# Performance work log

Hardware: AMD Instinct MI355X
Metric: run time of the kernel (lower is better)

The kernel has to match this reference:

```python
import jax, jax.numpy as jnp
import numpy as np

B, T, C, H = 4, 2048, 1024, 16
HD = C // H  # head dim = 64


def _rope(x, pos):
    """Rotary embedding. x: [B,H,T,hd], pos: [B,T] int positions."""
    half = x.shape[-1] // 2
    inv_freq = 1.0 / (10000.0 ** (jnp.arange(half, dtype=jnp.float32) / half))
    ang = pos.astype(jnp.float32)[:, None, :, None] * inv_freq  # [B,1,T,half]
    cos, sin = jnp.cos(ang), jnp.sin(ang)
    x1, x2 = x[..., :half], x[..., half:]
    return jnp.concatenate([x1 * cos - x2 * sin, x1 * sin + x2 * cos], axis=-1)


def setup_inputs() -> dict:
    key = jax.random.key(0)
    k1, k2, k3 = jax.random.split(key, 3)
    x = jax.random.normal(k1, (B, T, C), dtype=jnp.float32)
    W_attn = jax.random.normal(k2, (C, 3 * C), dtype=jnp.float32) * (1.0 / np.sqrt(C))
    W_proj = jax.random.normal(k3, (C, C), dtype=jnp.float32) * (1.0 / np.sqrt(C))
    indices = jnp.broadcast_to(jnp.arange(T, dtype=jnp.int32)[None, :], (B, T))
    return {"x": x, "W_attn": W_attn, "W_proj": W_proj, "indices": indices}


def reference(x, W_attn, W_proj, indices):
    # QKV projection (bias=False)
    qkv = x @ W_attn  # [B,T,3C]
    q, k, v = jnp.split(qkv, 3, axis=-1)

    def to_heads(t):
        return t.reshape(B, T, H, HD).transpose(0, 2, 1, 3)  # [B,H,T,hd]

    q, k, v = to_heads(q), to_heads(k), to_heads(v)
    # RoPE on q and k at positions given by indices (pos_emb_closure.adapt_*)
    q = _rope(q, indices)
    k = _rope(k, indices)

    # attn_mask = k_indices <= q_indices, shape [B,1,T,T]
    mask = indices[:, None, None, :] <= indices[:, None, :, None]

    att = jnp.einsum("bhqd,bhkd->bhqk", q, k) * (1.0 / np.sqrt(HD))
    att = jnp.where(mask, att, jnp.float32(-jnp.inf))
    att = jax.nn.softmax(att, axis=-1)
    y = jnp.einsum("bhqk,bhkd->bhqd", att, v)  # [B,H,T,hd]
    y = y.transpose(0, 2, 1, 3).reshape(B, T, C)
    return y @ W_proj
```

## Files before the change

kernel.cpp:

```cpp
#include <hip/hip_runtime.h>
#include <math.h>

namespace {
constexpr int Bsz = 4;
constexpr int T   = 2048;
constexpr int C   = 1024;
constexpr int H   = 16;
constexpr int HD  = 64;

typedef short bf16x8 __attribute__((ext_vector_type(8)));
typedef float f32x4  __attribute__((ext_vector_type(4)));
typedef unsigned int u32x4 __attribute__((ext_vector_type(4)));

#if defined(__has_builtin)
#if __has_builtin(__builtin_amdgcn_global_load_lds)
#define HAVE_GLL 1
typedef __attribute__((address_space(3))) unsigned int lds_u32_t;
typedef __attribute__((address_space(1))) unsigned int g_u32_t;
#define GLL16(gp, lp)                                                        \
  __builtin_amdgcn_global_load_lds((const g_u32_t*)(gp), (lds_u32_t*)(lp),   \
                                   16, 0, 0)
#endif
#endif

__device__ __forceinline__ unsigned short f2bf(float f) {
  unsigned int u = __builtin_bit_cast(unsigned int, f);
  u += 0x7FFFu + ((u >> 16) & 1u);
  return (unsigned short)(u >> 16);
}
__device__ __forceinline__ unsigned int cvtpk_bf16(float a, float b) {
  unsigned int r;
  asm("v_cvt_pk_bf16_f32 %0, %1, %2" : "=v"(r) : "v"(a), "v"(b));
  return r;
}

__global__ __launch_bounds__(256) void f32_to_bf16_kernel(
    const float* __restrict__ in, unsigned short* __restrict__ out, int n4) {
  int i = blockIdx.x * 256 + threadIdx.x;
  if (i < n4) {
    float4 v = ((const float4*)in)[i];
    ushort4 o;
    o.x = f2bf(v.x); o.y = f2bf(v.y); o.z = f2bf(v.z); o.w = f2bf(v.w);
    ((ushort4*)out)[i] = o;
  }
}

__global__ __launch_bounds__(256) void transpose_bf16_kernel(
    const float* __restrict__ W, unsigned short* __restrict__ Wt, int K, int N) {
  __shared__ float tile[32][33];
  const int n0 = blockIdx.x * 32, k0 = blockIdx.y * 32;
  const int r = threadIdx.x >> 3, c4 = threadIdx.x & 7;
  float4 v = *(const float4*)(W + (size_t)(k0 + r) * N + n0 + c4 * 4);
  tile[r][c4 * 4 + 0] = v.x;
  tile[r][c4 * 4 + 1] = v.y;
  tile[r][c4 * 4 + 2] = v.z;
  tile[r][c4 * 4 + 3] = v.w;
  __syncthreads();
  ushort4 o;
  o.x = f2bf(tile[c4 * 4 + 0][r]);
  o.y = f2bf(tile[c4 * 4 + 1][r]);
  o.z = f2bf(tile[c4 * 4 + 2][r]);
  o.w = f2bf(tile[c4 * 4 + 3][r]);
  *(ushort4*)(Wt + (size_t)(n0 + r) * K + k0 + c4 * 4) = o;
}

__global__ __launch_bounds__(256) void rope_table_kernel(
    const int* __restrict__ idx, float2* __restrict__ tab) {
  const int i = blockIdx.x * 256 + threadIdx.x;
  const int d = i & 31, g = i >> 5;
  const int pos = idx[g];
  const float inv = exp2f((float)d * -0.41524101186f);
  float sn, cs;
  sincosf((float)pos * inv, &sn, &cs);
  tab[i] = make_float2(cs, sn);
}

template <int MODE>
__global__ __launch_bounds__(256) void gemm_bt(
    const unsigned short* __restrict__ A, const unsigned short* __restrict__ Bt,
    float* __restrict__ Cout, unsigned short* __restrict__ qp,
    unsigned short* __restrict__ kp, unsigned short* __restrict__ vp,
    const float2* __restrict__ tab, int M, int N, int K) {
  __shared__ __align__(16) unsigned short As[128 * 32];
  __shared__ __align__(16) unsigned short Bs[128 * 32];
  const int tid = threadIdx.x;
  const int lane = tid & 63, w = tid >> 6;
  const int wr = w & 1, wc = w >> 1;
  const int l15 = lane & 15, quad = lane >> 4;
  const int m0 = blockIdx.y * 128, n0 = blockIdx.x * 128;

  const int srow = lane >> 2;
  const int schunk = (lane & 3) * 8;
  const unsigned short* gA = A + (size_t)(m0 + w * 32 + srow) * K + schunk;
  const unsigned short* gB = Bt + (size_t)(n0 + w * 32 + srow) * K + schunk;
  unsigned short* lA0 = &As[(w * 32) * 32 + lane * 8];
  unsigned short* lA1 = &As[(w * 32 + 16) * 32 + lane * 8];
  unsigned short* lB0 = &Bs[(w * 32) * 32 + lane * 8];
  unsigned short* lB1 = &Bs[(w * 32 + 16) * 32 + lane * 8];

  f32x4 acc[4][4] = {};

  for (int k0 = 0; k0 < K; k0 += 32) {
    __syncthreads();
#ifdef HAVE_GLL
    GLL16(gA + k0, lA0);
    GLL16(gA + (size_t)16 * K + k0, lA1);
    GLL16(gB + k0, lB0);
    GLL16(gB + (size_t)16 * K + k0, lB1);
#else
    *(uint4*)lA0 = *(const uint4*)(gA + k0);
    *(uint4*)lA1 = *(const uint4*)(gA + (size_t)16 * K + k0);
    *(uint4*)lB0 = *(const uint4*)(gB + k0);
    *(uint4*)lB1 = *(const uint4*)(gB + (size_t)16 * K + k0);
#endif
    __syncthreads();

    bf16x8 af[4], bfr[4];
#pragma unroll
    for (int mf = 0; mf < 4; ++mf)
      af[mf] = *(const bf16x8*)&As[(wr * 64 + mf * 16 + l15) * 32 + quad * 8];
#pragma unroll
    for (int nf = 0; nf < 4; ++nf)
      bfr[nf] = *(const bf16x8*)&Bs[(wc * 64 + nf * 16 + l15) * 32 + quad * 8];
#pragma unroll
    for (int mf = 0; mf < 4; ++mf)
#pragma unroll
      for (int nf = 0; nf < 4; ++nf)
        acc[mf][nf] = __builtin_amdgcn_mfma_f32_16x16x32_bf16(
            af[mf], bfr[nf], acc[mf][nf], 0, 0, 0);
  }

  if (MODE == 0) {
#pragma unroll
    for (int mf = 0; mf < 4; ++mf) {
      const int row0 = m0 + wr * 64 + mf * 16 + quad * 4;
#pragma unroll
      for (int nf = 0; nf < 4; ++nf) {
        const int col = n0 + wc * 64 + nf * 16 + l15;
#pragma unroll
        for (int r = 0; r < 4; ++r)
          Cout[(size_t)(row0 + r) * N + col] = acc[mf][nf][r];
      }
    }
  } else {
    const int colbase = n0 + wc * 64;
    const int which = colbase >> 10;
    if (which == 2) {
#pragma unroll
      for (int mf = 0; mf < 4; ++mf) {
        const int row0 = m0 + wr * 64 + mf * 16 + quad * 4;
        const int b = row0 >> 11, t0 = row0 & (T - 1);
#pragma unroll
        for (int nf = 0; nf < 4; ++nf) {
          const int rem = (colbase + nf * 16 + l15) & (C - 1);
          const int h = rem >> 6, hd = rem & 63;
          ushort4 pv;
          pv.x = f2bf(acc[mf][nf][0]);
          pv.y = f2bf(acc[mf][nf][1]);
          pv.z = f2bf(acc[mf][nf][2]);
          pv.w = f2bf(acc[mf][nf][3]);
          *(ushort4*)(vp + (((size_t)(b * H + h)) * HD + hd) * T + t0) = pv;
        }
      }
    } else {
      unsigned short* dst = (which == 0) ? qp : kp;
      const float sc = (which == 0) ? 0.18033688f : 1.0f;
      const int h = ((colbase + l15) & (C - 1)) >> 6;
#pragma unroll
      for (int mf = 0; mf < 4; ++mf) {
        const int row0 = m0 + wr * 64 + mf * 16 + quad * 4;
        const int b = row0 >> 11, t0 = row0 & (T - 1);
        const size_t obase = ((size_t)(b * H + h)) * T + t0;
        const float2* tb = tab + ((size_t)(b * T + t0) << 5);
#pragma unroll
        for (int nf = 0; nf < 2; ++nf) {
          const int d = nf * 16 + l15;
#pragma unroll
          for (int r = 0; r < 4; ++r) {
            const float2 cssn = tb[(r << 5) + d];
            const float x1 = acc[mf][nf][r], x2 = acc[mf][nf + 2][r];
            dst[(obase + r) * HD + d]      = f2bf((x1 * cssn.x - x2 * cssn.y) * sc);
            dst[(obase + r) * HD + d + 32] = f2bf((x1 * cssn.y + x2 * cssn.x) * sc);
          }
        }
      }
    }
  }
}

__global__ __launch_bounds__(256) void flash_attn_mfma(
    const unsigned short* __restrict__ q, const unsigned short* __restrict__ k,
    const unsigned short* __restrict__ vt, const int* __restrict__ idx,
    unsigned short* __restrict__ y) {
  __shared__ __align__(16) unsigned short Ks[2][64 * 64];
  __shared__ __align__(16) unsigned short Vts[2][64 * 64];

  const int tid = threadIdx.x;
  const int lane = tid & 63, w = tid >> 6;
  const int l15 = lane & 15, quad = lane >> 4;

  const int flat = (blockIdx.z * H + blockIdx.y) * 32 + blockIdx.x;
  const int slot = flat >> 3;
  const int bh_i = (flat & 7) * 8 + (slot >> 5);
  const int qt = 31 - (slot & 31);
  const int h = bh_i & (H - 1), b = bh_i >> 4;

  const size_t bh = (size_t)bh_i;
  const unsigned short* qg = q + bh * T * HD;
  const unsigned short* kg = k + bh * T * HD;
  const unsigned short* vg = vt + bh * HD * T;
  const int* idxb = idx + b * T;

  int km;
  {
    const int4* p4 = (const int4*)(idxb + (lane << 5));
    int4 v0 = p4[0];
    int m = max(max(v0.x, v0.y), max(v0.z, v0.w));
#pragma unroll
    for (int j = 1; j < 8; ++j) {
      int4 v = p4[j];
      m = max(m, max(max(v.x, v.y), max(v.z, v.w)));
    }
    km = max(m, __shfl_xor(m, 1));
  }

  const int r1 = tid >> 3, c1 = tid & 7;
  const int r2 = r1 + 32;
  const int xr1 = (r1 & 7) << 3;
  const int swS1 = r1 * 64 + ((c1 * 8) ^ xr1);
  const int swS2 = r2 * 64 + ((c1 * 8) ^ xr1);
  const int vbase = 32 * (c1 >> 2) + 16 * (c1 & 1) + 4 * ((c1 >> 1) & 1);
  const int vo1a = r1 * 64 + ((vbase + 0) ^ xr1);
  const int vo1b = r1 * 64 + ((vbase + 8) ^ xr1);
  const int vo2a = r2 * 64 + ((vbase + 0) ^ xr1);
  const int vo2b = r2 * 64 + ((vbase + 8) ^ xr1);
  const int rx = (l15 & 7) << 3;

  const int qrow = qt * 64 + w * 16 + l15;

  const bf16x8 bq0 = *(const bf16x8*)(qg + (size_t)qrow * HD + quad * 8);
  const bf16x8 bq1 = *(const bf16x8*)(qg + (size_t)qrow * HD + 32 + quad * 8);
  const int pq = idxb[qrow];
  int mq = pq;
  mq = min(mq, __shfl_xor(mq, 1));
  mq = min(mq, __shfl_xor(mq, 2));
  mq = min(mq, __shfl_xor(mq, 4));
  mq = min(mq, __shfl_xor(mq, 8));
  const unsigned long long bal = __ballot(km > mq);

  float m_run = -1e38f, lq = 0.0f;
  f32x4 Oa[4] = {};

  {
    uint4 ka = *(const uint4*)(kg + (size_t)r1 * HD + c1 * 8);
    uint4 kb = *(const uint4*)(kg + (size_t)r2 * HD + c1 * 8);
    uint4 va = *(const uint4*)(vg + (size_t)r1 * T + c1 * 8);
    uint4 vb = *(const uint4*)(vg + (size_t)r2 * T + c1 * 8);
    *(uint4*)&Ks[0][swS1] = ka;
    *(uint4*)&Ks[0][swS2] = kb;
    *(uint2*)&Vts[0][vo1a] = make_uint2(va.x, va.y);
    *(uint2*)&Vts[0][vo1b] = make_uint2(va.z, va.w);
    *(uint2*)&Vts[0][vo2a] = make_uint2(vb.x, vb.y);
    *(uint2*)&Vts[0][vo2b] = make_uint2(vb.z, vb.w);
  }

  for (int kt = 0; kt <= qt; ++kt) {
    const int cur = kt & 1;
    const int k0 = kt * 64;
    __syncthreads();

    uint4 nka, nkb, nva, nvb;
    if (kt < qt) {
      const int kn = k0 + 64;
      nka = *(const uint4*)(kg + (size_t)(kn + r1) * HD + c1 * 8);
      nkb = *(const uint4*)(kg + (size_t)(kn + r2) * HD + c1 * 8);
      nva = *(const uint4*)(vg + (size_t)r1 * T + kn + c1 * 8);
      nvb = *(const uint4*)(vg + (size_t)r2 * T + kn + c1 * 8);
    }

    f32x4 Sa[4];
    __builtin_amdgcn_s_setprio(1);
#pragma unroll
    for (int nf = 0; nf < 4; ++nf) {
      const int row = (nf * 16 + l15) * 64;
      bf16x8 ak0 = *(const bf16x8*)&Ks[cur][row + ((quad * 8) ^ rx)];
      bf16x8 ak1 = *(const bf16x8*)&Ks[cur][row + ((32 + quad * 8) ^ rx)];
      f32x4 s = {};
      s = __builtin_amdgcn_mfma_f32_16x16x32_bf16(ak0, bq0, s, 0, 0, 0);
      s = __builtin_amdgcn_mfma_f32_16x16x32_bf16(ak1, bq1, s, 0, 0, 0);
      Sa[nf] = s;
    }
    __builtin_amdgcn_s_setprio(0);

    if ((bal >> (kt + kt)) & 1ull) {
#pragma unroll
      for (int nf = 0; nf < 4; ++nf) {
        const int4 pk4 = *(const int4*)(idxb + k0 + nf * 16 + quad * 4);
        if (pk4.x > pq) Sa[nf][0] = -3e38f;
        if (pk4.y > pq) Sa[nf][1] = -3e38f;
        if (pk4.z > pq) Sa[nf][2] = -3e38f;
        if (pk4.w > pq) Sa[nf][3] = -3e38f;
      }
    }

    float mx = fmaxf(
        fmaxf(fmaxf(fmaxf(Sa[0][0], Sa[0][1]), Sa[0][2]),
              fmaxf(fmaxf(Sa[0][3], Sa[1][0]), Sa[1][1])),
        fmaxf(fmaxf(fmaxf(Sa[1][2], Sa[1][3]), Sa[2][0]),
              fmaxf(fmaxf(Sa[2][1], Sa[2][2]), Sa[2][3])));
    mx = fmaxf(mx, fmaxf(fmaxf(Sa[3][0], Sa[3][1]), fmaxf(Sa[3][2], Sa[3][3])));
    mx = fmaxf(mx, __shfl_xor(mx, 16));
    mx = fmaxf(mx, __shfl_xor(mx, 32));

    if (!__all(mx <= m_run + 8.0f)) {
      const float mn = fmaxf(m_run, mx);
      const float alpha = exp2f(m_run - mn);
      m_run = mn;
      lq *= alpha;
#pragma unroll
      for (int nfd = 0; nfd < 4; ++nfd)
#pragma unroll
        for (int r = 0; r < 4; ++r) Oa[nfd][r] *= alpha;
    }

    u32x4 w0, w1;
#pragma unroll
    for (int nf = 0; nf < 4; ++nf) {
      float p0 = exp2f(Sa[nf][0] - m_run);
      float p1 = exp2f(Sa[nf][1] - m_run);
      float p2 = exp2f(Sa[nf][2] - m_run);
      float p3 = exp2f(Sa[nf][3] - m_run);
      Sa[nf][0] = p0; Sa[nf][1] = p1; Sa[nf][2] = p2; Sa[nf][3] = p3;
      if (nf < 2) {
        w0[nf * 2 + 0] = cvtpk_bf16(p0, p1);
        w0[nf * 2 + 1] = cvtpk_bf16(p2, p3);
      } else {
        w1[(nf - 2) * 2 + 0] = cvtpk_bf16(p0, p1);
        w1[(nf - 2) * 2 + 1] = cvtpk_bf16(p2, p3);
      }
    }
    const bf16x8 bp0 = __builtin_bit_cast(bf16x8, w0);
    const bf16x8 bp1 = __builtin_bit_cast(bf16x8, w1);

    __builtin_amdgcn_s_setprio(1);
#pragma unroll
    for (int nfd = 0; nfd < 4; ++nfd) {
      const int vrow = (nfd * 16 + l15) * 64;
      bf16x8 av0 = *(const bf16x8*)&Vts[cur][vrow + ((quad * 8) ^ rx)];
      bf16x8 av1 = *(const bf16x8*)&Vts[cur][vrow + ((32 + quad * 8) ^ rx)];
      Oa[nfd] = __builtin_amdgcn_mfma_f32_16x16x32_bf16(av0, bp0, Oa[nfd], 0, 0, 0);
      Oa[nfd] = __builtin_amdgcn_mfma_f32_16x16x32_bf16(av1, bp1, Oa[nfd], 0, 0, 0);
    }
    __builtin_amdgcn_s_setprio(0);

    lq += ((Sa[0][0] + Sa[0][1]) + (Sa[0][2] + Sa[0][3])) +
          ((Sa[1][0] + Sa[1][1]) + (Sa[1][2] + Sa[1][3])) +
          ((Sa[2][0] + Sa[2][1]) + (Sa[2][2] + Sa[2][3])) +
          ((Sa[3][0] + Sa[3][1]) + (Sa[3][2] + Sa[3][3]));

    if (kt < qt) {
      const int nxt = cur ^ 1;
      *(uint4*)&Ks[nxt][swS1] = nka;
      *(uint4*)&Ks[nxt][swS2] = nkb;
      *(uint2*)&Vts[nxt][vo1a] = make_uint2(nva.x, nva.y);
      *(uint2*)&Vts[nxt][vo1b] = make_uint2(nva.z, nva.w);
      *(uint2*)&Vts[nxt][vo2a] = make_uint2(nvb.x, nvb.y);
      *(uint2*)&Vts[nxt][vo2b] = make_uint2(nvb.z, nvb.w);
    }
  }

  float lsum = lq;
  lsum += __shfl_xor(lsum, 16);
  lsum += __shfl_xor(lsum, 32);
  const float rl = 1.0f / lsum;
  const size_t base = ((size_t)b * T + qrow) * (size_t)C + h * HD;
#pragma unroll
  for (int nfd = 0; nfd < 4; ++nfd) {
    ushort4 o;
    o.x = f2bf(Oa[nfd][0] * rl);
    o.y = f2bf(Oa[nfd][1] * rl);
    o.z = f2bf(Oa[nfd][2] * rl);
    o.w = f2bf(Oa[nfd][3] * rl);
    *(ushort4*)(y + base + nfd * 16 + quad * 4) = o;
  }
}

}

extern "C" void kernel_launch(void* const* d_in, const int* in_sizes, int n_in,
                              void* d_out, int out_size, void* d_ws,
                              size_t ws_size, hipStream_t stream) {
  const float* x      = (const float*)d_in[0];
  const float* W_attn = (const float*)d_in[1];
  const float* W_proj = (const float*)d_in[2];
  const int* indices  = (const int*)d_in[3];
  float* out = (float*)d_out;

  const size_t nM = (size_t)Bsz * T * C;
  unsigned short* xb  = (unsigned short*)d_ws;
  unsigned short* wat = xb + nM;
  unsigned short* wpt = wat + (size_t)3 * C * C;
  unsigned short* qp  = wpt + (size_t)C * C;
  unsigned short* kp  = qp + nM;
  unsigned short* vp  = kp + nM;
  unsigned short* yb  = vp + nM;
  float2* rtab = (float2*)(yb + nM);

  f32_to_bf16_kernel<<<(int)(nM / 4 / 256), 256, 0, stream>>>(x, xb, (int)(nM / 4));
  transpose_bf16_kernel<<<dim3(3 * C / 32, C / 32), 256, 0, stream>>>(W_attn, wat, C, 3 * C);
  transpose_bf16_kernel<<<dim3(C / 32, C / 32), 256, 0, stream>>>(W_proj, wpt, C, C);
  rope_table_kernel<<<(Bsz * T * 32) / 256, 256, 0, stream>>>(indices, rtab);
  gemm_bt<1><<<dim3(3 * C / 128, Bsz * T / 128), 256, 0, stream>>>(
      xb, wat, nullptr, qp, kp, vp, rtab, Bsz * T, 3 * C, C);
  flash_attn_mfma<<<dim3(32, H, Bsz), 256, 0, stream>>>(qp, kp, vp, indices, yb);
  gemm_bt<0><<<dim3(C / 128, Bsz * T / 128), 256, 0, stream>>>(
      yb, wpt, out, nullptr, nullptr, nullptr, nullptr, Bsz * T, C, C);
}
```

Before: 310.9 us.

## Load K fragments directly from global into registers, bypassing LDS

In the attention kernel, K tiles are no longer staged through shared memory. Each wave now loads its MFMA K operand fragments straight from global memory into registers and prefetches the next tile into a second register set. This removes the K LDS writes and reads and halves LDS usage. In exchange, every one of the four waves loads the full K tile separately, four times the global/L2 traffic for K, and register pressure rises by 16 extra VGPRs per set.

```diff
diff --git a/kernel.cpp b/kernel.cpp
--- a/kernel.cpp
+++ b/kernel.cpp
@@ -192,7 +192,6 @@
     const unsigned short* __restrict__ q, const unsigned short* __restrict__ k,
     const unsigned short* __restrict__ vt, const int* __restrict__ idx,
     unsigned short* __restrict__ y) {
-  __shared__ __align__(16) unsigned short Ks[2][64 * 64];
   __shared__ __align__(16) unsigned short Vts[2][64 * 64];
 
   const int tid = threadIdx.x;
@@ -227,8 +226,6 @@
   const int r1 = tid >> 3, c1 = tid & 7;
   const int r2 = r1 + 32;
   const int xr1 = (r1 & 7) << 3;
-  const int swS1 = r1 * 64 + ((c1 * 8) ^ xr1);
-  const int swS2 = r2 * 64 + ((c1 * 8) ^ xr1);
   const int vbase = 32 * (c1 >> 2) + 16 * (c1 & 1) + 4 * ((c1 >> 1) & 1);
   const int vo1a = r1 * 64 + ((vbase + 0) ^ xr1);
   const int vo1b = r1 * 64 + ((vbase + 8) ^ xr1);
@@ -248,16 +245,20 @@
   mq = min(mq, __shfl_xor(mq, 8));
   const unsigned long long bal = __ballot(km > mq);
 
+  const unsigned short* kfb = kg + (size_t)l15 * HD + quad * 8;
+
   float m_run = -1e38f, lq = 0.0f;
   f32x4 Oa[4] = {};
 
+  bf16x8 kc[8];
   {
-    uint4 ka = *(const uint4*)(kg + (size_t)r1 * HD + c1 * 8);
-    uint4 kb = *(const uint4*)(kg + (size_t)r2 * HD + c1 * 8);
+#pragma unroll
+    for (int nf = 0; nf < 4; ++nf) {
+      kc[nf * 2 + 0] = *(const bf16x8*)(kfb + (size_t)(nf * 16) * HD);
+      kc[nf * 2 + 1] = *(const bf16x8*)(kfb + (size_t)(nf * 16) * HD + 32);
+    }
     uint4 va = *(const uint4*)(vg + (size_t)r1 * T + c1 * 8);
     uint4 vb = *(const uint4*)(vg + (size_t)r2 * T + c1 * 8);
-    *(uint4*)&Ks[0][swS1] = ka;
-    *(uint4*)&Ks[0][swS2] = kb;
     *(uint2*)&Vts[0][vo1a] = make_uint2(va.x, va.y);
     *(uint2*)&Vts[0][vo1b] = make_uint2(va.z, va.w);
     *(uint2*)&Vts[0][vo2a] = make_uint2(vb.x, vb.y);
@@ -269,25 +270,27 @@
     const int k0 = kt * 64;
     __syncthreads();
 
-    uint4 nka, nkb, nva, nvb;
+    bf16x8 kn[8];
+    uint4 nva, nvb;
     if (kt < qt) {
-      const int kn = k0 + 64;
-      nka = *(const uint4*)(kg + (size_t)(kn + r1) * HD + c1 * 8);
-      nkb = *(const uint4*)(kg + (size_t)(kn + r2) * HD + c1 * 8);
-      nva = *(const uint4*)(vg + (size_t)r1 * T + kn + c1 * 8);
-      nvb = *(const uint4*)(vg + (size_t)r2 * T + kn + c1 * 8);
+      const int knext0 = k0 + 64;
+      const unsigned short* kfn = kfb + (size_t)knext0 * HD;
+#pragma unroll
+      for (int nf = 0; nf < 4; ++nf) {
+        kn[nf * 2 + 0] = *(const bf16x8*)(kfn + (size_t)(nf * 16) * HD);
+        kn[nf * 2 + 1] = *(const bf16x8*)(kfn + (size_t)(nf * 16) * HD + 32);
+      }
+      nva = *(const uint4*)(vg + (size_t)r1 * T + knext0 + c1 * 8);
+      nvb = *(const uint4*)(vg + (size_t)r2 * T + knext0 + c1 * 8);
     }
 
     f32x4 Sa[4];
     __builtin_amdgcn_s_setprio(1);
 #pragma unroll
     for (int nf = 0; nf < 4; ++nf) {
-      const int row = (nf * 16 + l15) * 64;
-      bf16x8 ak0 = *(const bf16x8*)&Ks[cur][row + ((quad * 8) ^ rx)];
-      bf16x8 ak1 = *(const bf16x8*)&Ks[cur][row + ((32 + quad * 8) ^ rx)];
       f32x4 s = {};
-      s = __builtin_amdgcn_mfma_f32_16x16x32_bf16(ak0, bq0, s, 0, 0, 0);
-      s = __builtin_amdgcn_mfma_f32_16x16x32_bf16(ak1, bq1, s, 0, 0, 0);
+      s = __builtin_amdgcn_mfma_f32_16x16x32_bf16(kc[nf * 2 + 0], bq0, s, 0, 0, 0);
+      s = __builtin_amdgcn_mfma_f32_16x16x32_bf16(kc[nf * 2 + 1], bq1, s, 0, 0, 0);
       Sa[nf] = s;
     }
     __builtin_amdgcn_s_setprio(0);
@@ -360,12 +363,12 @@
 
     if (kt < qt) {
       const int nxt = cur ^ 1;
-      *(uint4*)&Ks[nxt][swS1] = nka;
-      *(uint4*)&Ks[nxt][swS2] = nkb;
       *(uint2*)&Vts[nxt][vo1a] = make_uint2(nva.x, nva.y);
       *(uint2*)&Vts[nxt][vo1b] = make_uint2(nva.z, nva.w);
       *(uint2*)&Vts[nxt][vo2a] = make_uint2(nvb.x, nvb.y);
       *(uint2*)&Vts[nxt][vo2b] = make_uint2(nvb.z, nvb.w);
+#pragma unroll
+      for (int i = 0; i < 8; ++i) kc[i] = kn[i];
     }
   }
 
```

New measurement: 397.0 us. 27.7% more time.

## Process two 64-key tiles per iteration in flash attention loop

Applied to the files above, without the earlier changes.

The attention inner loop now handles 128 keys per iteration, two 64-wide subtiles sharing one barrier, one online-softmax max/rescale step, and one double-buffered prefetch of the next two tiles. Prefetch loads are issued after the QK and softmax max stage instead of at loop start. The aim is to halve barriers and rescale checks per key and to expose more independent MFMA work. The cost is double the LDS footprint (64KB), more live registers, and partial waste when qt is even and the second subtile is absent.

```diff
diff --git a/kernel.cpp b/kernel.cpp
--- a/kernel.cpp
+++ b/kernel.cpp
@@ -192,8 +192,8 @@
     const unsigned short* __restrict__ q, const unsigned short* __restrict__ k,
     const unsigned short* __restrict__ vt, const int* __restrict__ idx,
     unsigned short* __restrict__ y) {
-  __shared__ __align__(16) unsigned short Ks[2][64 * 64];
-  __shared__ __align__(16) unsigned short Vts[2][64 * 64];
+  __shared__ __align__(16) unsigned short Ks[2][128 * 64];
+  __shared__ __align__(16) unsigned short Vts[2][128 * 64];
 
   const int tid = threadIdx.x;
   const int lane = tid & 63, w = tid >> 6;
@@ -252,33 +252,29 @@
   f32x4 Oa[4] = {};
 
   {
-    uint4 ka = *(const uint4*)(kg + (size_t)r1 * HD + c1 * 8);
-    uint4 kb = *(const uint4*)(kg + (size_t)r2 * HD + c1 * 8);
-    uint4 va = *(const uint4*)(vg + (size_t)r1 * T + c1 * 8);
-    uint4 vb = *(const uint4*)(vg + (size_t)r2 * T + c1 * 8);
-    *(uint4*)&Ks[0][swS1] = ka;
-    *(uint4*)&Ks[0][swS2] = kb;
-    *(uint2*)&Vts[0][vo1a] = make_uint2(va.x, va.y);
-    *(uint2*)&Vts[0][vo1b] = make_uint2(va.z, va.w);
-    *(uint2*)&Vts[0][vo2a] = make_uint2(vb.x, vb.y);
-    *(uint2*)&Vts[0][vo2b] = make_uint2(vb.z, vb.w);
-  }
-
-  for (int kt = 0; kt <= qt; ++kt) {
-    const int cur = kt & 1;
-    const int k0 = kt * 64;
+#pragma unroll
+    for (int hf = 0; hf < 2; ++hf) {
+      const int kb = hf * 64;
+      uint4 ka = *(const uint4*)(kg + (size_t)(kb + r1) * HD + c1 * 8);
+      uint4 kx = *(const uint4*)(kg + (size_t)(kb + r2) * HD + c1 * 8);
+      uint4 va = *(const uint4*)(vg + (size_t)r1 * T + kb + c1 * 8);
+      uint4 vb = *(const uint4*)(vg + (size_t)r2 * T + kb + c1 * 8);
+      *(uint4*)&Ks[0][hf * 4096 + swS1] = ka;
+      *(uint4*)&Ks[0][hf * 4096 + swS2] = kx;
+      *(uint2*)&Vts[0][hf * 4096 + vo1a] = make_uint2(va.x, va.y);
+      *(uint2*)&Vts[0][hf * 4096 + vo1b] = make_uint2(va.z, va.w);
+      *(uint2*)&Vts[0][hf * 4096 + vo2a] = make_uint2(vb.x, vb.y);
+      *(uint2*)&Vts[0][hf * 4096 + vo2b] = make_uint2(vb.z, vb.w);
+    }
+  }
+
+  for (int kt = 0; kt <= qt; kt += 2) {
+    const int cur = (kt >> 1) & 1;
+    const bool hasB = (kt + 1) <= qt;
+    const bool pf = (kt + 2) <= qt;
     __syncthreads();
 
-    uint4 nka, nkb, nva, nvb;
-    if (kt < qt) {
-      const int kn = k0 + 64;
-      nka = *(const uint4*)(kg + (size_t)(kn + r1) * HD + c1 * 8);
-      nkb = *(const uint4*)(kg + (size_t)(kn + r2) * HD + c1 * 8);
-      nva = *(const uint4*)(vg + (size_t)r1 * T + kn + c1 * 8);
-      nvb = *(const uint4*)(vg + (size_t)r2 * T + kn + c1 * 8);
-    }
-
-    f32x4 Sa[4];
+    f32x4 SaA[4], SaB[4];
     __builtin_amdgcn_s_setprio(1);
 #pragma unroll
     for (int nf = 0; nf < 4; ++nf) {
@@ -288,27 +284,58 @@
       f32x4 s = {};
       s = __builtin_amdgcn_mfma_f32_16x16x32_bf16(ak0, bq0, s, 0, 0, 0);
       s = __builtin_amdgcn_mfma_f32_16x16x32_bf16(ak1, bq1, s, 0, 0, 0);
-      Sa[nf] = s;
+      SaA[nf] = s;
+    }
+    if (hasB) {
+#pragma unroll
+      for (int nf = 0; nf < 4; ++nf) {
+        const int row = 4096 + (nf * 16 + l15) * 64;
+        bf16x8 ak0 = *(const bf16x8*)&Ks[cur][row + ((quad * 8) ^ rx)];
+        bf16x8 ak1 = *(const bf16x8*)&Ks[cur][row + ((32 + quad * 8) ^ rx)];
+        f32x4 s = {};
+        s = __builtin_amdgcn_mfma_f32_16x16x32_bf16(ak0, bq0, s, 0, 0, 0);
+        s = __builtin_amdgcn_mfma_f32_16x16x32_bf16(ak1, bq1, s, 0, 0, 0);
+        SaB[nf] = s;
+      }
     }
     __builtin_amdgcn_s_setprio(0);
 
     if ((bal >> (kt + kt)) & 1ull) {
 #pragma unroll
       for (int nf = 0; nf < 4; ++nf) {
-        const int4 pk4 = *(const int4*)(idxb + k0 + nf * 16 + quad * 4);
-        if (pk4.x > pq) Sa[nf][0] = -3e38f;
-        if (pk4.y > pq) Sa[nf][1] = -3e38f;
-        if (pk4.z > pq) Sa[nf][2] = -3e38f;
-        if (pk4.w > pq) Sa[nf][3] = -3e38f;
+        const int4 pk4 = *(const int4*)(idxb + kt * 64 + nf * 16 + quad * 4);
+        if (pk4.x > pq) SaA[nf][0] = -3e38f;
+        if (pk4.y > pq) SaA[nf][1] = -3e38f;
+        if (pk4.z > pq) SaA[nf][2] = -3e38f;
+        if (pk4.w > pq) SaA[nf][3] = -3e38f;
+      }
+    }
+    if (hasB && ((bal >> (kt + kt + 2)) & 1ull)) {
+#pragma unroll
+      for (int nf = 0; nf < 4; ++nf) {
+        const int4 pk4 = *(const int4*)(idxb + (kt + 1) * 64 + nf * 16 + quad * 4);
+        if (pk4.x > pq) SaB[nf][0] = -3e38f;
+        if (pk4.y > pq) SaB[nf][1] = -3e38f;
+        if (pk4.z > pq) SaB[nf][2] = -3e38f;
+        if (pk4.w > pq) SaB[nf][3] = -3e38f;
       }
     }
 
     float mx = fmaxf(
-        fmaxf(fmaxf(fmaxf(Sa[0][0], Sa[0][1]), Sa[0][2]),
-              fmaxf(fmaxf(Sa[0][3], Sa[1][0]), Sa[1][1])),
-        fmaxf(fmaxf(fmaxf(Sa[1][2], Sa[1][3]), Sa[2][0]),
-              fmaxf(fmaxf(Sa[2][1], Sa[2][2]), Sa[2][3])));
-    mx = fmaxf(mx, fmaxf(fmaxf(Sa[3][0], Sa[3][1]), fmaxf(Sa[3][2], Sa[3][3])));
+        fmaxf(fmaxf(fmaxf(SaA[0][0], SaA[0][1]), SaA[0][2]),
+              fmaxf(fmaxf(SaA[0][3], SaA[1][0]), SaA[1][1])),
+        fmaxf(fmaxf(fmaxf(SaA[1][2], SaA[1][3]), SaA[2][0]),
+              fmaxf(fmaxf(SaA[2][1], SaA[2][2]), SaA[2][3])));
+    mx = fmaxf(mx, fmaxf(fmaxf(SaA[3][0], SaA[3][1]), fmaxf(SaA[3][2], SaA[3][3])));
+    if (hasB) {
+      float mb = fmaxf(
+          fmaxf(fmaxf(fmaxf(SaB[0][0], SaB[0][1]), SaB[0][2]),
+                fmaxf(fmaxf(SaB[0][3], SaB[1][0]), SaB[1][1])),
+          fmaxf(fmaxf(fmaxf(SaB[1][2], SaB[1][3]), SaB[2][0]),
+                fmaxf(fmaxf(SaB[2][1], SaB[2][2]), SaB[2][3])));
+      mb = fmaxf(mb, fmaxf(fmaxf(SaB[3][0], SaB[3][1]), fmaxf(SaB[3][2], SaB[3][3])));
+      mx = fmaxf(mx, mb);
+    }
     mx = fmaxf(mx, __shfl_xor(mx, 16));
     mx = fmaxf(mx, __shfl_xor(mx, 32));
 
@@ -323,49 +350,96 @@
         for (int r = 0; r < 4; ++r) Oa[nfd][r] *= alpha;
     }
 
-    u32x4 w0, w1;
-#pragma unroll
-    for (int nf = 0; nf < 4; ++nf) {
-      float p0 = exp2f(Sa[nf][0] - m_run);
-      float p1 = exp2f(Sa[nf][1] - m_run);
-      float p2 = exp2f(Sa[nf][2] - m_run);
-      float p3 = exp2f(Sa[nf][3] - m_run);
-      Sa[nf][0] = p0; Sa[nf][1] = p1; Sa[nf][2] = p2; Sa[nf][3] = p3;
-      if (nf < 2) {
-        w0[nf * 2 + 0] = cvtpk_bf16(p0, p1);
-        w0[nf * 2 + 1] = cvtpk_bf16(p2, p3);
-      } else {
-        w1[(nf - 2) * 2 + 0] = cvtpk_bf16(p0, p1);
-        w1[(nf - 2) * 2 + 1] = cvtpk_bf16(p2, p3);
-      }
-    }
-    const bf16x8 bp0 = __builtin_bit_cast(bf16x8, w0);
-    const bf16x8 bp1 = __builtin_bit_cast(bf16x8, w1);
-
-    __builtin_amdgcn_s_setprio(1);
-#pragma unroll
-    for (int nfd = 0; nfd < 4; ++nfd) {
-      const int vrow = (nfd * 16 + l15) * 64;
-      bf16x8 av0 = *(const bf16x8*)&Vts[cur][vrow + ((quad * 8) ^ rx)];
-      bf16x8 av1 = *(const bf16x8*)&Vts[cur][vrow + ((32 + quad * 8) ^ rx)];
-      Oa[nfd] = __builtin_amdgcn_mfma_f32_16x16x32_bf16(av0, bp0, Oa[nfd], 0, 0, 0);
-      Oa[nfd] = __builtin_amdgcn_mfma_f32_16x16x32_bf16(av1, bp1, Oa[nfd], 0, 0, 0);
-    }
-    __builtin_amdgcn_s_setprio(0);
-
-    lq += ((Sa[0][0] + Sa[0][1]) + (Sa[0][2] + Sa[0][3])) +
-          ((Sa[1][0] + Sa[1][1]) + (Sa[1][2] + Sa[1][3])) +
-          ((Sa[2][0] + Sa[2][1]) + (Sa[2][2] + Sa[2][3])) +
-          ((Sa[3][0] + Sa[3][1]) + (Sa[3][2] + Sa[3][3]));
-
-    if (kt < qt) {
+    uint4 nk[4], nv[4];
+    if (pf) {
+#pragma unroll
+      for (int hf = 0; hf < 2; ++hf) {
+        const int kb = (kt + 2 + hf) * 64;
+        nk[hf * 2 + 0] = *(const uint4*)(kg + (size_t)(kb + r1) * HD + c1 * 8);
+        nk[hf * 2 + 1] = *(const uint4*)(kg + (size_t)(kb + r2) * HD + c1 * 8);
+        nv[hf * 2 + 0] = *(const uint4*)(vg + (size_t)r1 * T + kb + c1 * 8);
+        nv[hf * 2 + 1] = *(const uint4*)(vg + (size_t)r2 * T + kb + c1 * 8);
+      }
+    }
+
+    {
+      float s0 = 0.f, s1 = 0.f, s2 = 0.f, s3 = 0.f;
+      u32x4 w0, w1;
+#pragma unroll
+      for (int nf = 0; nf < 4; ++nf) {
+        float p0 = exp2f(SaA[nf][0] - m_run);
+        float p1 = exp2f(SaA[nf][1] - m_run);
+        float p2 = exp2f(SaA[nf][2] - m_run);
+        float p3 = exp2f(SaA[nf][3] - m_run);
+        s0 += p0; s1 += p1; s2 += p2; s3 += p3;
+        if (nf < 2) {
+          w0[nf * 2 + 0] = cvtpk_bf16(p0, p1);
+          w0[nf * 2 + 1] = cvtpk_bf16(p2, p3);
+        } else {
+          w1[(nf - 2) * 2 + 0] = cvtpk_bf16(p0, p1);
+          w1[(nf - 2) * 2 + 1] = cvtpk_bf16(p2, p3);
+        }
+      }
+      lq += (s0 + s1) + (s2 + s3);
+      const bf16x8 bp0 = __builtin_bit_cast(bf16x8, w0);
+      const bf16x8 bp1 = __builtin_bit_cast(bf16x8, w1);
+      __builtin_amdgcn_s_setprio(1);
+#pragma unroll
+      for (int nfd = 0; nfd < 4; ++nfd) {
+        const int vrow = (nfd * 16 + l15) * 64;
+        bf16x8 av0 = *(const bf16x8*)&Vts[cur][vrow + ((quad * 8) ^ rx)];
+        bf16x8 av1 = *(const bf16x8*)&Vts[cur][vrow + ((32 + quad * 8) ^ rx)];
+        Oa[nfd] = __builtin_amdgcn_mfma_f32_16x16x32_bf16(av0, bp0, Oa[nfd], 0, 0, 0);
+        Oa[nfd] = __builtin_amdgcn_mfma_f32_16x16x32_bf16(av1, bp1, Oa[nfd], 0, 0, 0);
+      }
+      __builtin_amdgcn_s_setprio(0);
+    }
+
+    if (hasB) {
+      float s0 = 0.f, s1 = 0.f, s2 = 0.f, s3 = 0.f;
+      u32x4 w0, w1;
+#pragma unroll
+      for (int nf = 0; nf < 4; ++nf) {
+        float p0 = exp2f(SaB[nf][0] - m_run);
+        float p1 = exp2f(SaB[nf][1] - m_run);
+        float p2 = exp2f(SaB[nf][2] - m_run);
+        float p3 = exp2f(SaB[nf][3] - m_run);
+        s0 += p0; s1 += p1; s2 += p2; s3 += p3;
+        if (nf < 2) {
+          w0[nf * 2 + 0] = cvtpk_bf16(p0, p1);
+          w0[nf * 2 + 1] = cvtpk_bf16(p2, p3);
+        } else {
+          w1[(nf - 2) * 2 + 0] = cvtpk_bf16(p0, p1);
+          w1[(nf - 2) * 2 + 1] = cvtpk_bf16(p2, p3);
+        }
+      }
+      lq += (s0 + s1) + (s2 + s3);
+      const bf16x8 bp0 = __builtin_bit_cast(bf16x8, w0);
+      const bf16x8 bp1 = __builtin_bit_cast(bf16x8, w1);
+      __builtin_amdgcn_s_setprio(1);
+#pragma unroll
+      for (int nfd = 0; nfd < 4; ++nfd) {
+        const int vrow = 4096 + (nfd * 16 + l15) * 64;
+        bf16x8 av0 = *(const bf16x8*)&Vts[cur][vrow + ((quad * 8) ^ rx)];
+        bf16x8 av1 = *(const bf16x8*)&Vts[cur][vrow + ((32 + quad * 8) ^ rx)];
+        Oa[nfd] = __builtin_amdgcn_mfma_f32_16x16x32_bf16(av0, bp0, Oa[nfd], 0, 0, 0);
+        Oa[nfd] = __builtin_amdgcn_mfma_f32_16x16x32_bf16(av1, bp1, Oa[nfd], 0, 0, 0);
+      }
+      __builtin_amdgcn_s_setprio(0);
+    }
+
+    if (pf) {
       const int nxt = cur ^ 1;
-      *(uint4*)&Ks[nxt][swS1] = nka;
-      *(uint4*)&Ks[nxt][swS2] = nkb;
-      *(uint2*)&Vts[nxt][vo1a] = make_uint2(nva.x, nva.y);
-      *(uint2*)&Vts[nxt][vo1b] = make_uint2(nva.z, nva.w);
-      *(uint2*)&Vts[nxt][vo2a] = make_uint2(nvb.x, nvb.y);
-      *(uint2*)&Vts[nxt][vo2b] = make_uint2(nvb.z, nvb.w);
+#pragma unroll
+      for (int hf = 0; hf < 2; ++hf) {
+        *(uint4*)&Ks[nxt][hf * 4096 + swS1] = nk[hf * 2 + 0];
+        *(uint4*)&Ks[nxt][hf * 4096 + swS2] = nk[hf * 2 + 1];
+        const uint4 va = nv[hf * 2 + 0], vb = nv[hf * 2 + 1];
+        *(uint2*)&Vts[nxt][hf * 4096 + vo1a] = make_uint2(va.x, va.y);
+        *(uint2*)&Vts[nxt][hf * 4096 + vo1b] = make_uint2(va.z, va.w);
+        *(uint2*)&Vts[nxt][hf * 4096 + vo2a] = make_uint2(vb.x, vb.y);
+        *(uint2*)&Vts[nxt][hf * 4096 + vo2b] = make_uint2(vb.z, vb.w);
+      }
     }
   }
 
```

New measurement: 344.0 us. 1.11x slower.
